# Kernel tuning notes

Hardware: AMD Instinct MI355X
Metric: run time of the kernel (lower is better)

## Reference

```python
import jax, jax.numpy as jnp
import numpy as np

HEAD_SIZE = 64
NUM_HEADS = 8
D_IN = 512

def setup_inputs() -> dict:
    key = jax.random.key(0)
    ks = jax.random.split(key, 6)
    B, Nq, Nk = 4, 2048, 2048
    HD = HEAD_SIZE * NUM_HEADS
    q = jax.random.normal(ks[0], (B, Nq, D_IN), dtype=jnp.float32)
    k = jax.random.normal(ks[1], (B, Nk, D_IN), dtype=jnp.float32)
    s = 1.0 / np.sqrt(D_IN)
    Wq = jax.random.normal(ks[2], (D_IN, HD), dtype=jnp.float32) * s
    Wk = jax.random.normal(ks[3], (D_IN, HD), dtype=jnp.float32) * s
    Wv = jax.random.normal(ks[4], (D_IN, HD), dtype=jnp.float32) * s
    Wh = jax.random.normal(ks[5], (HD, HEAD_SIZE), dtype=jnp.float32) * (1.0 / np.sqrt(HD))
    return {"q": q, "k": k, "Wq": Wq, "Wk": Wk, "Wv": Wv, "Wh": Wh}

def reference(q, k, Wq, Wk, Wv, Wh):
    B, Nq, _ = q.shape
    Nk = k.shape[1]
    H, hs = NUM_HEADS, HEAD_SIZE
    # QKV projections (no bias), reshape to [B, H, N, hs]
    q_ = (q @ Wq).reshape(B, Nq, H, hs).transpose(0, 2, 1, 3)
    k_ = (k @ Wk).reshape(B, Nk, H, hs).transpose(0, 2, 1, 3)
    v_ = (k @ Wv).reshape(B, Nk, H, hs).transpose(0, 2, 1, 3)
    scale = 1.0 / jnp.sqrt(jnp.float32(hs))
    score = jnp.einsum('bhqd,bhkd->bhqk', q_, k_) * scale  # [B,H,Nq,Nk]
    attn = jax.nn.softmax(score, axis=-1)
    wv = jnp.einsum('bhqk,bhkd->bhqd', attn, v_)  # [B,H,Nq,hs]
    wv = wv.transpose(0, 2, 1, 3).reshape(B, Nq, H * hs)
    return wv @ Wh  # [B, Nq, hs]
```

## Files before the change

kernel.cpp:

```cpp
#include <hip/hip_runtime.h>
#include <hip/hip_bf16.h>

#define BB   4
#define NQ   2048
#define NKK  2048
#define DIN  512
#define NH   8
#define HS   64
#define HD   512

typedef __hip_bfloat16 bf16;
typedef unsigned short ushort_t;
typedef __attribute__((ext_vector_type(8))) short short8;
typedef __attribute__((ext_vector_type(4))) float f32x4;
typedef __attribute__((ext_vector_type(16))) float f32x16;
typedef __attribute__((ext_vector_type(4))) unsigned u32x4;

__device__ __forceinline__ unsigned short f2bu(float x) {
  bf16 h = __float2bfloat16(x);
  return *(unsigned short*)&h;
}

__global__ __launch_bounds__(256) void wtrans_kernel(
    const float* __restrict__ Wq, const float* __restrict__ Wk,
    const float* __restrict__ Wv, const float* __restrict__ Wh,
    ushort_t* __restrict__ Wt, ushort_t* __restrict__ Wht) {
  const int z = blockIdx.z;
  const float* src;
  ushort_t* dst;
  int S;
  if (z < 3) {
    src = (z == 0) ? Wq : (z == 1) ? Wk : Wv;
    dst = Wt + (size_t)z * 512 * 512;
    S = 512;
  } else {
    if (blockIdx.y != 0) return;
    src = Wh;
    dst = Wht;
    S = 64;
  }
  const int k0 = blockIdx.x * 64;
  const int n0 = (z < 3) ? blockIdx.y * 64 : 0;

  __shared__ ushort_t Ls[64 * 72];
  const int tid = threadIdx.x;
  {
    int r = tid >> 2, cb = (tid & 3) * 16;
    const float* sp = src + (size_t)(k0 + r) * S + n0 + cb;
#pragma unroll
    for (int ii = 0; ii < 4; ++ii) {
      float4 f = *(const float4*)(sp + ii * 4);
      __align__(8) ushort_t t4[4] = {f2bu(f.x), f2bu(f.y), f2bu(f.z), f2bu(f.w)};
      *(uint2*)(&Ls[r * 72 + cb + ii * 4]) = *(uint2*)t4;
    }
  }
  __syncthreads();
  {
    int rr = tid >> 2, tb = (tid & 3) * 16;
    __align__(16) ushort_t tmp[16];
#pragma unroll
    for (int j = 0; j < 16; ++j) tmp[j] = Ls[(tb + j) * 72 + rr];
    ushort_t* dp = dst + (size_t)(n0 + rr) * 512 + k0 + tb;
    *(int4*)dp       = ((int4*)tmp)[0];
    *(int4*)(dp + 8) = ((int4*)tmp)[1];
  }
}

__global__ __launch_bounds__(256) void proj_kernel(
    const float* __restrict__ q, const float* __restrict__ k,
    const ushort_t* __restrict__ Wt, ushort_t* __restrict__ Qf,
    ushort_t* __restrict__ Kf, ushort_t* __restrict__ Vf) {
  const int z = blockIdx.z;
  const float* X = (z == 0) ? q : k;
  const ushort_t* Wz = Wt + (size_t)z * 512 * 512;
  ushort_t* Y = (z == 0) ? Qf : (z == 1) ? Kf : Vf;
  const float sc = (z == 0) ? 0.18033688011112042f : 1.0f;

  __shared__ ushort_t As[2 * 128 * 40];
  __shared__ ushort_t Bs[2 * 128 * 40];

  const int tid  = threadIdx.x;
  const int lane = tid & 63;
  const int w    = tid >> 6;
  const int quad = lane >> 4;
  const int c    = lane & 15;
  const int wm   = w >> 1, wn = w & 1;

  const int m0 = blockIdx.y * 128;
  const int n0 = blockIdx.x * 128;
  const int sm  = tid >> 1;
  const int skb = (tid & 1) * 16;

  float4 xa[4];
  int4 wb[2];
  auto load_t = [&](int k0) {
    const float* xp = X + (size_t)(m0 + sm) * DIN + k0 + skb;
    xa[0] = *(const float4*)(xp + 0);
    xa[1] = *(const float4*)(xp + 4);
    xa[2] = *(const float4*)(xp + 8);
    xa[3] = *(const float4*)(xp + 12);
    const ushort_t* wp = Wz + (size_t)(n0 + sm) * 512 + k0 + skb;
    wb[0] = *(const int4*)wp;
    wb[1] = *(const int4*)(wp + 8);
  };
  auto store_t = [&](int buf) {
    __align__(16) ushort_t ta[16];
#pragma unroll
    for (int ii = 0; ii < 4; ++ii) {
      ta[ii * 4 + 0] = f2bu(xa[ii].x);
      ta[ii * 4 + 1] = f2bu(xa[ii].y);
      ta[ii * 4 + 2] = f2bu(xa[ii].z);
      ta[ii * 4 + 3] = f2bu(xa[ii].w);
    }
    *(int4*)(&As[buf * 5120 + sm * 40 + skb])     = ((int4*)ta)[0];
    *(int4*)(&As[buf * 5120 + sm * 40 + skb + 8]) = ((int4*)ta)[1];
    *(int4*)(&Bs[buf * 5120 + sm * 40 + skb])     = wb[0];
    *(int4*)(&Bs[buf * 5120 + sm * 40 + skb + 8]) = wb[1];
  };

  f32x4 acc[4][4];
#pragma unroll
  for (int m = 0; m < 4; ++m)
#pragma unroll
    for (int n = 0; n < 4; ++n) acc[m][n] = (f32x4)0.0f;

  load_t(0);
  store_t(0);
  __syncthreads();

  for (int t = 0; t < 16; ++t) {
    const int cur = t & 1;
    if (t < 15) load_t((t + 1) * 32);
    const ushort_t* as = As + cur * 5120;
    const ushort_t* bs = Bs + cur * 5120;
    short8 af[4], bfr[4];
#pragma unroll
    for (int m = 0; m < 4; ++m)
      af[m] = *(const short8*)(&as[(wm * 64 + m * 16 + c) * 40 + quad * 8]);
#pragma unroll
    for (int n = 0; n < 4; ++n)
      bfr[n] = *(const short8*)(&bs[(wn * 64 + n * 16 + c) * 40 + quad * 8]);
#pragma unroll
    for (int m = 0; m < 4; ++m)
#pragma unroll
      for (int n = 0; n < 4; ++n)
        acc[m][n] = __builtin_amdgcn_mfma_f32_16x16x32_bf16(af[m], bfr[n], acc[m][n], 0, 0, 0);
    if (t < 15) store_t(cur ^ 1);
    __syncthreads();
  }

#pragma unroll
  for (int m = 0; m < 4; ++m)
#pragma unroll
    for (int n = 0; n < 4; ++n)
#pragma unroll
      for (int r = 0; r < 4; ++r) {
        int row = m0 + wm * 64 + m * 16 + quad * 4 + r;
        int col = n0 + wn * 64 + n * 16 + c;
        Y[(size_t)row * HD + col] = f2bu(acc[m][n][r] * sc);
      }
}

__global__ __launch_bounds__(256) void vtrans_kernel(
    const ushort_t* __restrict__ Vf, ushort_t* __restrict__ Vt) {
  const int b  = blockIdx.z;
  const int t0 = blockIdx.x * 64;
  const int c0 = blockIdx.y * 64;
  __shared__ ushort_t Ls[64 * 72];
  const int tid = threadIdx.x;
  {
    int r = tid >> 2, cb = (tid & 3) * 16;
    const ushort_t* src = Vf + (size_t)(b * NQ + t0 + r) * HD + c0 + cb;
    *(int4*)(&Ls[r * 72 + cb])     = *(const int4*)src;
    *(int4*)(&Ls[r * 72 + cb + 8]) = *(const int4*)(src + 8);
  }
  __syncthreads();
  {
    int rr = tid >> 2, tb = (tid & 3) * 16;
    __align__(16) ushort_t tmp[16];
#pragma unroll
    for (int j = 0; j < 16; ++j) tmp[j] = Ls[(tb + j) * 72 + rr];
    ushort_t* dst = Vt + (size_t)(b * HD + c0 + rr) * NKK + t0 + tb;
    *(int4*)dst       = ((int4*)tmp)[0];
    *(int4*)(dst + 8) = ((int4*)tmp)[1];
  }
}

__global__ __launch_bounds__(128) void attn_kernel(
    const ushort_t* __restrict__ Qf, const ushort_t* __restrict__ Kf,
    const ushort_t* __restrict__ Vt, ushort_t* __restrict__ CTX) {
  const int qb = blockIdx.x;
  const int h  = blockIdx.y;
  const int b  = blockIdx.z;

  __shared__ ushort_t Kt[2 * 64 * 64];
  __shared__ ushort_t Vs[2 * 64 * 64];

  const int tid  = threadIdx.x;
  const int lane = tid & 63;
  const int w    = tid >> 6;
  const int ql   = lane & 31;
  const int hi   = lane >> 5;

  const int q0 = qb * 128 + w * 64;

  short8 bq[2][4];
#pragma unroll
  for (int qs = 0; qs < 2; ++qs) {
    const ushort_t* qp =
        Qf + (size_t)(b * NQ + q0 + qs * 32 + ql) * HD + h * HS + hi * 8;
#pragma unroll
    for (int ks = 0; ks < 4; ++ks) bq[qs][ks] = *(const short8*)(qp + ks * 16);
  }

  const int sub  = lane >> 3;
  const int slot = lane & 7;
  const int csrc = slot ^ sub;
  const ushort_t* kp0 =
      Kf + (size_t)(b * NKK + w * 32 + sub) * HD + h * HS + csrc * 8;
  const ushort_t* vp0 =
      Vt + (size_t)((b * NH + h) * HS + w * 32 + sub) * NKK + csrc * 8;

  auto stage = [&](int buf, int kt) {
    const ushort_t* kp = kp0 + (size_t)kt * 64 * HD;
    const ushort_t* vp = vp0 + (size_t)kt * 64;
#pragma unroll
    for (int i = 0; i < 4; ++i) {
      __builtin_amdgcn_global_load_lds(
          (const __attribute__((address_space(1))) unsigned*)(kp + (size_t)i * 8 * HD),
          (__attribute__((address_space(3))) unsigned*)(&Kt[buf * 4096 + (w * 4 + i) * 512]),
          16, 0, 0);
      __builtin_amdgcn_global_load_lds(
          (const __attribute__((address_space(1))) unsigned*)(vp + (size_t)i * 8 * NKK),
          (__attribute__((address_space(3))) unsigned*)(&Vs[buf * 4096 + (w * 4 + i) * 512]),
          16, 0, 0);
    }
  };

  f32x16 o[2][2];
#pragma unroll
  for (int qs = 0; qs < 2; ++qs)
#pragma unroll
    for (int ng = 0; ng < 2; ++ng) o[qs][ng] = (f32x16)0.0f;
  float lsum[2] = {0.0f, 0.0f};

  stage(0, 0);
  __syncthreads();

  for (int kt = 0; kt < NKK / 64; ++kt) {
    const int cur = kt & 1;
    if (kt < NKK / 64 - 1) stage(cur ^ 1, kt + 1);
    const ushort_t* kb = &Kt[cur * 4096];
    const ushort_t* vb = &Vs[cur * 4096];

#pragma unroll
    for (int kg = 0; kg < 2; ++kg) {
      f32x16 s[2];
      s[0] = (f32x16)0.0f;
      s[1] = (f32x16)0.0f;
      const int krow = kg * 32 + ql;
      __builtin_amdgcn_s_setprio(1);
#pragma unroll
      for (int ks = 0; ks < 4; ++ks) {
        short8 ak = *(const short8*)(&kb[krow * 64 + (((ks * 2 + hi) ^ (krow & 7)) * 8)]);
        s[0] = __builtin_amdgcn_mfma_f32_32x32x16_bf16(ak, bq[0][ks], s[0], 0, 0, 0);
        s[1] = __builtin_amdgcn_mfma_f32_32x32x16_bf16(ak, bq[1][ks], s[1], 0, 0, 0);
      }
      __builtin_amdgcn_s_setprio(0);

      short8 pa[2][2];
#pragma unroll
      for (int qs = 0; qs < 2; ++qs) {
        float p[16];
#pragma unroll
        for (int r = 0; r < 16; ++r) p[r] = __builtin_amdgcn_exp2f(s[qs][r]);
        {
          float a0 = p[0] + p[1], a1 = p[2] + p[3], a2 = p[4] + p[5], a3 = p[6] + p[7];
          float a4 = p[8] + p[9], a5 = p[10] + p[11], a6 = p[12] + p[13], a7 = p[14] + p[15];
          a0 += a1; a2 += a3; a4 += a5; a6 += a7;
          lsum[qs] += (a0 + a2) + (a4 + a6);
        }
#pragma unroll
        for (int sp = 0; sp < 2; ++sp) {
          unsigned wA, wB, wC, wD;
          asm("v_cvt_pk_bf16_f32 %0, %1, %2" : "=v"(wA) : "v"(p[8 * sp + 0]), "v"(p[8 * sp + 1]));
          asm("v_cvt_pk_bf16_f32 %0, %1, %2" : "=v"(wB) : "v"(p[8 * sp + 2]), "v"(p[8 * sp + 3]));
          asm("v_cvt_pk_bf16_f32 %0, %1, %2" : "=v"(wC) : "v"(p[8 * sp + 4]), "v"(p[8 * sp + 5]));
          asm("v_cvt_pk_bf16_f32 %0, %1, %2" : "=v"(wD) : "v"(p[8 * sp + 6]), "v"(p[8 * sp + 7]));
          asm("v_permlane32_swap_b32 %0, %1" : "+v"(wA), "+v"(wC));
          asm("v_permlane32_swap_b32 %0, %1" : "+v"(wB), "+v"(wD));
          u32x4 pw;
          pw.x = wA;
          pw.y = wB;
          pw.z = wC;
          pw.w = wD;
          pa[qs][sp] = __builtin_bit_cast(short8, pw);
        }
      }

      __builtin_amdgcn_s_setprio(1);
#pragma unroll
      for (int sp = 0; sp < 2; ++sp) {
        const int ks = kg * 2 + sp;
#pragma unroll
        for (int ng = 0; ng < 2; ++ng) {
          const int vrow = ng * 32 + ql;
          short8 bv = *(const short8*)(&vb[vrow * 64 + (((ks * 2 + hi) ^ (vrow & 7)) * 8)]);
          o[0][ng] = __builtin_amdgcn_mfma_f32_32x32x16_bf16(pa[0][sp], bv, o[0][ng], 0, 0, 0);
          o[1][ng] = __builtin_amdgcn_mfma_f32_32x32x16_bf16(pa[1][sp], bv, o[1][ng], 0, 0, 0);
        }
      }
      __builtin_amdgcn_s_setprio(0);
    }

    __syncthreads();
  }

  float inv[2];
#pragma unroll
  for (int qs = 0; qs < 2; ++qs) {
    float tot = lsum[qs] + __shfl_xor(lsum[qs], 32);
    inv[qs] = 1.0f / tot;
  }

#pragma unroll
  for (int qs = 0; qs < 2; ++qs)
#pragma unroll
    for (int r = 0; r < 16; ++r) {
      int qr = (r & 3) + 8 * (r >> 2) + 4 * hi;
      float iv = __shfl(inv[qs], qr);
      size_t base = (size_t)(b * NQ + q0 + qs * 32 + qr) * HD + h * HS + ql;
      CTX[base]      = f2bu(o[qs][0][r] * iv);
      CTX[base + 32] = f2bu(o[qs][1][r] * iv);
    }
}

__global__ __launch_bounds__(64) void outproj_kernel(
    const ushort_t* __restrict__ CTX, const ushort_t* __restrict__ Wht,
    float* __restrict__ out) {
  const int lane = threadIdx.x & 63;
  const int quad = lane >> 4, c = lane & 15;
  const int m0 = blockIdx.x * 16;

  f32x4 o[4];
#pragma unroll
  for (int n = 0; n < 4; ++n) o[n] = (f32x4)0.0f;

  const ushort_t* arow = CTX + (size_t)(m0 + c) * HD;
#pragma unroll 4
  for (int ks = 0; ks < 16; ++ks) {
    short8 a = *(const short8*)(arow + ks * 32 + quad * 8);
#pragma unroll
    for (int nd = 0; nd < 4; ++nd) {
      short8 bn = *(const short8*)(Wht + (size_t)(nd * 16 + c) * 512 + ks * 32 + quad * 8);
      o[nd] = __builtin_amdgcn_mfma_f32_16x16x32_bf16(a, bn, o[nd], 0, 0, 0);
    }
  }
#pragma unroll
  for (int nd = 0; nd < 4; ++nd)
#pragma unroll
    for (int r = 0; r < 4; ++r)
      out[(size_t)(m0 + quad * 4 + r) * HS + nd * 16 + c] = o[nd][r];
}

extern "C" void kernel_launch(void* const* d_in, const int* in_sizes, int n_in,
                              void* d_out, int out_size, void* d_ws,
                              size_t ws_size, hipStream_t stream) {
  const float* q  = (const float*)d_in[0];
  const float* k  = (const float*)d_in[1];
  const float* Wq = (const float*)d_in[2];
  const float* Wk = (const float*)d_in[3];
  const float* Wv = (const float*)d_in[4];
  const float* Wh = (const float*)d_in[5];
  float* out = (float*)d_out;

  const size_t E = (size_t)BB * NQ * HD;
  ushort_t* ws  = (ushort_t*)d_ws;
  ushort_t* Qf  = ws;
  ushort_t* Kf  = Qf + E;
  ushort_t* Vt  = Kf + E;
  ushort_t* CTX = Vt + E;
  ushort_t* Vf  = CTX + E;
  ushort_t* Wt  = Vf + E;
  ushort_t* Wht = Wt + (size_t)3 * 512 * 512;

  wtrans_kernel<<<dim3(8, 8, 4), 256, 0, stream>>>(Wq, Wk, Wv, Wh, Wt, Wht);
  proj_kernel<<<dim3(HD / 128, BB * NQ / 128, 3), 256, 0, stream>>>(
      q, k, Wt, Qf, Kf, Vf);
  vtrans_kernel<<<dim3(NKK / 64, HD / 64, BB), 256, 0, stream>>>(Vf, Vt);
  attn_kernel<<<dim3(NQ / 128, NH, BB), 128, 0, stream>>>(Qf, Kf, Vt, CTX);
  outproj_kernel<<<dim3(BB * NQ / 16), 64, 0, stream>>>(CTX, Wht, out);
}
```

Baseline: 202.9 us.

## Split key range across two wave pairs in attention block and merge via LDS

The attention block grows from 2 to 4 waves. Each pair of waves processes half of the key/value sequence against the same 64 queries, using its own double-buffered K/V tiles in LDS. At the end, the second half writes its partial output accumulators and row sums into shared memory. The first half then adds them, normalizes and stores the context. This halves the serial key loop per wave and doubles the waves resident per CU to hide memory and MFMA latency. In exchange it adds an LDS reduction step and uses more shared memory per block.

```diff
diff --git a/kernel.cpp b/kernel.cpp
--- a/kernel.cpp
+++ b/kernel.cpp
@@ -186,40 +186,42 @@
   }
 }
 
-__global__ __launch_bounds__(128) void attn_kernel(
+__global__ __launch_bounds__(256) void attn_kernel(
     const ushort_t* __restrict__ Qf, const ushort_t* __restrict__ Kf,
     const ushort_t* __restrict__ Vt, ushort_t* __restrict__ CTX) {
   const int qb = blockIdx.x;
   const int h  = blockIdx.y;
   const int b  = blockIdx.z;
 
-  __shared__ ushort_t Kt[2 * 64 * 64];
-  __shared__ ushort_t Vs[2 * 64 * 64];
+  __shared__ ushort_t Kt[2][2][4096];
+  __shared__ ushort_t Vs[2][2][4096];
 
   const int tid  = threadIdx.x;
   const int lane = tid & 63;
   const int w    = tid >> 6;
+  const int qp   = w & 1;
+  const int kh   = w >> 1;
   const int ql   = lane & 31;
   const int hi   = lane >> 5;
 
-  const int q0 = qb * 128 + w * 64;
+  const int q0 = qb * 128 + qp * 64;
 
   short8 bq[2][4];
 #pragma unroll
   for (int qs = 0; qs < 2; ++qs) {
-    const ushort_t* qp =
+    const ushort_t* qp_ =
         Qf + (size_t)(b * NQ + q0 + qs * 32 + ql) * HD + h * HS + hi * 8;
 #pragma unroll
-    for (int ks = 0; ks < 4; ++ks) bq[qs][ks] = *(const short8*)(qp + ks * 16);
+    for (int ks = 0; ks < 4; ++ks) bq[qs][ks] = *(const short8*)(qp_ + ks * 16);
   }
 
   const int sub  = lane >> 3;
   const int slot = lane & 7;
   const int csrc = slot ^ sub;
   const ushort_t* kp0 =
-      Kf + (size_t)(b * NKK + w * 32 + sub) * HD + h * HS + csrc * 8;
+      Kf + (size_t)(b * NKK + qp * 32 + sub) * HD + h * HS + csrc * 8;
   const ushort_t* vp0 =
-      Vt + (size_t)((b * NH + h) * HS + w * 32 + sub) * NKK + csrc * 8;
+      Vt + (size_t)((b * NH + h) * HS + qp * 32 + sub) * NKK + csrc * 8;
 
   auto stage = [&](int buf, int kt) {
     const ushort_t* kp = kp0 + (size_t)kt * 64 * HD;
@@ -228,11 +230,11 @@
     for (int i = 0; i < 4; ++i) {
       __builtin_amdgcn_global_load_lds(
           (const __attribute__((address_space(1))) unsigned*)(kp + (size_t)i * 8 * HD),
-          (__attribute__((address_space(3))) unsigned*)(&Kt[buf * 4096 + (w * 4 + i) * 512]),
+          (__attribute__((address_space(3))) unsigned*)(&Kt[kh][buf][(qp * 4 + i) * 512]),
           16, 0, 0);
       __builtin_amdgcn_global_load_lds(
           (const __attribute__((address_space(1))) unsigned*)(vp + (size_t)i * 8 * NKK),
-          (__attribute__((address_space(3))) unsigned*)(&Vs[buf * 4096 + (w * 4 + i) * 512]),
+          (__attribute__((address_space(3))) unsigned*)(&Vs[kh][buf][(qp * 4 + i) * 512]),
           16, 0, 0);
     }
   };
@@ -244,14 +246,14 @@
     for (int ng = 0; ng < 2; ++ng) o[qs][ng] = (f32x16)0.0f;
   float lsum[2] = {0.0f, 0.0f};
 
-  stage(0, 0);
+  stage(0, kh * 16);
   __syncthreads();
 
-  for (int kt = 0; kt < NKK / 64; ++kt) {
-    const int cur = kt & 1;
-    if (kt < NKK / 64 - 1) stage(cur ^ 1, kt + 1);
-    const ushort_t* kb = &Kt[cur * 4096];
-    const ushort_t* vb = &Vs[cur * 4096];
+  for (int t = 0; t < 16; ++t) {
+    const int cur = t & 1;
+    if (t < 15) stage(cur ^ 1, kh * 16 + t + 1);
+    const ushort_t* kb = &Kt[kh][cur][0];
+    const ushort_t* vb = &Vs[kh][cur][0];
 
 #pragma unroll
     for (int kg = 0; kg < 2; ++kg) {
@@ -316,23 +318,44 @@
     __syncthreads();
   }
 
-  float inv[2];
-#pragma unroll
-  for (int qs = 0; qs < 2; ++qs) {
-    float tot = lsum[qs] + __shfl_xor(lsum[qs], 32);
-    inv[qs] = 1.0f / tot;
-  }
-
-#pragma unroll
-  for (int qs = 0; qs < 2; ++qs)
-#pragma unroll
-    for (int r = 0; r < 16; ++r) {
-      int qr = (r & 3) + 8 * (r >> 2) + 4 * hi;
-      float iv = __shfl(inv[qs], qr);
-      size_t base = (size_t)(b * NQ + q0 + qs * 32 + qr) * HD + h * HS + ql;
-      CTX[base]      = f2bu(o[qs][0][r] * iv);
-      CTX[base + 32] = f2bu(o[qs][1][r] * iv);
-    }
+  float ls[2];
+#pragma unroll
+  for (int qs = 0; qs < 2; ++qs) ls[qs] = lsum[qs] + __shfl_xor(lsum[qs], 32);
+
+  float* S  = (float*)&Kt[0][0][0];
+  float* SL = (float*)&Vs[0][0][0];
+
+  if (kh == 1) {
+#pragma unroll
+    for (int qs = 0; qs < 2; ++qs) {
+#pragma unroll
+      for (int r = 0; r < 16; ++r) {
+        const int qr = (r & 3) + 8 * (r >> 2) + 4 * hi;
+        S[(qp * 64 + qs * 32 + qr) * 64 + ql]      = o[qs][0][r];
+        S[(qp * 64 + qs * 32 + qr) * 64 + 32 + ql] = o[qs][1][r];
+      }
+      if (hi == 0) SL[(qp * 2 + qs) * 32 + ql] = ls[qs];
+    }
+  }
+  __syncthreads();
+  if (kh == 0) {
+    float inv[2];
+#pragma unroll
+    for (int qs = 0; qs < 2; ++qs)
+      inv[qs] = 1.0f / (ls[qs] + SL[(qp * 2 + qs) * 32 + ql]);
+
+#pragma unroll
+    for (int qs = 0; qs < 2; ++qs)
+#pragma unroll
+      for (int r = 0; r < 16; ++r) {
+        const int qr = (r & 3) + 8 * (r >> 2) + 4 * hi;
+        float iv = __shfl(inv[qs], qr);
+        const float* srow = &S[(qp * 64 + qs * 32 + qr) * 64];
+        size_t base = (size_t)(b * NQ + q0 + qs * 32 + qr) * HD + h * HS + ql;
+        CTX[base]      = f2bu((o[qs][0][r] + srow[ql])      * iv);
+        CTX[base + 32] = f2bu((o[qs][1][r] + srow[32 + ql]) * iv);
+      }
+  }
 }
 
 __global__ __launch_bounds__(64) void outproj_kernel(
@@ -388,6 +411,6 @@
   proj_kernel<<<dim3(HD / 128, BB * NQ / 128, 3), 256, 0, stream>>>(
       q, k, Wt, Qf, Kf, Vf);
   vtrans_kernel<<<dim3(NKK / 64, HD / 64, BB), 256, 0, stream>>>(Vf, Vt);
-  attn_kernel<<<dim3(NQ / 128, NH, BB), 128, 0, stream>>>(Qf, Kf, Vt, CTX);
+  attn_kernel<<<dim3(NQ / 128, NH, BB), 256, 0, stream>>>(Qf, Kf, Vt, CTX);
   outproj_kernel<<<dim3(BB * NQ / 16), 64, 0, stream>>>(CTX, Wht, out);
 }
```

Result: slower. 212.3 us (+4.6%).
